# Kernel optimization log

Hardware: AMD Instinct MI355X
Metric: run time of the kernel (lower is better)

Reference implementation:

```python
import jax, jax.numpy as jnp
import numpy as np

DIM = 4096
N_HEADS = 32
N_KV_HEADS = 8
HEAD_DIM = DIM // N_HEADS  # 128
N_REP = N_HEADS // N_KV_HEADS  # 4
THETA = 10000.0
B, S = 4, 1024


def setup_inputs() -> dict:
    key = jax.random.key(0)
    ks = jax.random.split(key, 5)
    sc = 1.0 / np.sqrt(DIM).astype(np.float32)
    x = jax.random.normal(ks[0], (B, S, DIM), jnp.float32)
    wq = jax.random.normal(ks[1], (DIM, N_HEADS * HEAD_DIM), jnp.float32) * sc
    wk = jax.random.normal(ks[2], (DIM, N_KV_HEADS * HEAD_DIM), jnp.float32) * sc
    wv = jax.random.normal(ks[3], (DIM, N_KV_HEADS * HEAD_DIM), jnp.float32) * sc
    wo = jax.random.normal(ks[4], (N_HEADS * HEAD_DIM, DIM), jnp.float32) * sc
    return {"x": x, "wq": wq, "wk": wk, "wv": wv, "wo": wo}


def _rope_cos_sin(seq_len):
    # matches precompute_freqs_cis: freqs over even indices, angles = t * freqs
    freqs = 1.0 / (THETA ** (jnp.arange(0, HEAD_DIM, 2, dtype=jnp.float32) / HEAD_DIM))
    t = jnp.arange(seq_len, dtype=jnp.float32)
    ang = jnp.outer(t, freqs)  # [S, HEAD_DIM//2]
    return jnp.cos(ang), jnp.sin(ang)


def _apply_rope(x, cos, sin):
    # x: [B, S, H, D]; consecutive pairs form complex numbers (view_as_complex)
    xr = x[..., 0::2]
    xi = x[..., 1::2]
    c = cos[None, :, None, :]
    s = sin[None, :, None, :]
    out_r = xr * c - xi * s
    out_i = xr * s + xi * c
    return jnp.stack([out_r, out_i], axis=-1).reshape(x.shape)


def reference(x, wq, wk, wv, wo):
    bsz, seq_len, _ = x.shape
    q = (x @ wq).reshape(bsz, seq_len, N_HEADS, HEAD_DIM)
    k = (x @ wk).reshape(bsz, seq_len, N_KV_HEADS, HEAD_DIM)
    v = (x @ wv).reshape(bsz, seq_len, N_KV_HEADS, HEAD_DIM)
    cos, sin = _rope_cos_sin(seq_len)
    q = _apply_rope(q, cos, sin)
    k = _apply_rope(k, cos, sin)
    # repeat_kv: expand each kv head N_REP times contiguously
    k = jnp.repeat(k, N_REP, axis=2)
    v = jnp.repeat(v, N_REP, axis=2)
    scores = jnp.einsum('bqhd,bkhd->bhqk', q, k) / np.float32(np.sqrt(HEAD_DIM))
    mask = jnp.triu(jnp.full((seq_len, seq_len), -jnp.inf, dtype=scores.dtype), k=1)
    scores = scores + mask
    attn = jax.nn.softmax(scores.astype(jnp.float32), axis=-1).astype(q.dtype)
    out = jnp.einsum('bhqk,bkhd->bqhd', attn, v).reshape(bsz, seq_len, N_HEADS * HEAD_DIM)
    return out @ wo
```

## Files before the change

### kernel.cpp

```cpp
#include <hip/hip_runtime.h>

typedef unsigned short u16;
typedef unsigned int u32;
typedef __attribute__((ext_vector_type(8))) short short8_t;
typedef __attribute__((ext_vector_type(4))) float f32x4;

static constexpr int Bc = 4, Sc = 1024, Hc = 32, HKVc = 8, Dc = 128;
static constexpr int BS = Bc * Sc;
static constexpr int DIMc = 4096;

__device__ __forceinline__ u16 f2bf(float f) {
  u32 u = __float_as_uint(f);
  u32 r = (u + 0x7fffu + ((u >> 16) & 1u)) >> 16;
  return (u16)r;
}
__device__ __forceinline__ float bf2f(u16 u) {
  return __uint_as_float(((u32)u) << 16);
}
__device__ __forceinline__ void gload_lds16(const void* g, void* l) {
  __builtin_amdgcn_global_load_lds((const __attribute__((address_space(1))) void*)g,
                                   (__attribute__((address_space(3))) void*)l, 16, 0, 0);
}

#define SBAR __builtin_amdgcn_sched_barrier(0)
#define PBARRIER do { SBAR; __builtin_amdgcn_s_barrier(); SBAR; } while (0)
#define WAITVM(N) asm volatile("s_waitcnt vmcnt(" #N ")" ::: "memory")

__global__ void rope_table_k(float* __restrict__ tbl) {
  int i = blockIdx.x * 256 + threadIdx.x;
  int s = i >> 6, fi = i & 63;
  float freq = powf(10000.f, -(float)fi / 64.f);
  float ang = (float)s * freq;
  float sv, cv;
  sincosf(ang, &sv, &cv);
  tbl[2 * i] = cv;
  tbl[2 * i + 1] = sv;
}

__global__ void f32_to_bf16_k(const float* __restrict__ in, u16* __restrict__ out, int n4) {
  int i = blockIdx.x * 256 + threadIdx.x;
  if (i >= n4) return;
  float4 v = *(const float4*)(in + (size_t)i * 4);
  uint2 pk;
  pk.x = (u32)f2bf(v.x) | ((u32)f2bf(v.y) << 16);
  pk.y = (u32)f2bf(v.z) | ((u32)f2bf(v.w) << 16);
  *(uint2*)(out + (size_t)i * 4) = pk;
}

__global__ __launch_bounds__(256) void transpose_w_k(const float* __restrict__ W, u16* __restrict__ WT,
                                                     int Kdim, int Ndim) {
  __shared__ float tile[64 * 65];
  const int t = threadIdx.x;
  const int n0 = blockIdx.x * 64, k0 = blockIdx.y * 64;
  #pragma unroll
  for (int p = 0; p < 4; ++p) {
    int idx = p * 256 + t;
    int r = idx >> 4, c = (idx & 15) * 4;
    float4 v = *(const float4*)(W + (size_t)(k0 + r) * Ndim + n0 + c);
    tile[r * 65 + c + 0] = v.x;
    tile[r * 65 + c + 1] = v.y;
    tile[r * 65 + c + 2] = v.z;
    tile[r * 65 + c + 3] = v.w;
  }
  __syncthreads();
  #pragma unroll
  for (int p = 0; p < 2; ++p) {
    int idx = p * 256 + t;
    int n = idx >> 3, c = (idx & 7) * 8;
    alignas(16) u16 o[8];
    #pragma unroll
    for (int i = 0; i < 8; ++i) o[i] = f2bf(tile[(c + i) * 65 + n]);
    *(uint4*)(WT + (size_t)(n0 + n) * Kdim + k0 + c) = *(const uint4*)o;
  }
}

#define MFMAQ(QI, AF, BF)                                                                \
  do {                                                                                   \
    __builtin_amdgcn_s_setprio(1);                                                       \
    _Pragma("unroll") for (int mf = 0; mf < 4; ++mf)                                     \
      _Pragma("unroll") for (int nf = 0; nf < 2; ++nf)                                   \
        _Pragma("unroll") for (int kk = 0; kk < 2; ++kk)                                 \
          acc[QI][mf][nf] = __builtin_amdgcn_mfma_f32_16x16x32_bf16(                     \
              AF[mf][kk], BF[nf][kk], acc[QI][mf][nf], 0, 0, 0);                         \
    __builtin_amdgcn_s_setprio(0);                                                       \
  } while (0)

template <int MODE>
__global__ __launch_bounds__(512, 2) void gemm256(const u16* __restrict__ A, const u16* __restrict__ BT,
                                                  void* __restrict__ Cv, const float* __restrict__ tbl,
                                                  int M, int N, int K) {
  extern __shared__ char smem[];
  const int t = threadIdx.x, l = t & 63, w = t >> 6;
  const int ln15 = l & 15, lh = l >> 4;
  const int NT = K >> 6;

  int id = blockIdx.x;
  int nwg = gridDim.x;
  int swz = ((nwg & 7) == 0) ? ((id & 7) * (nwg >> 3) + (id >> 3)) : id;
  const int nbn = N >> 8;
  const int bm = swz / nbn, bn = swz % nbn;

  const u16* Ag = A + (size_t)bm * 256 * K;
  const u16* Bg = BT + (size_t)bn * 256 * K;

  f32x4 acc[4][4][2];
  #pragma unroll
  for (int q = 0; q < 4; ++q)
    #pragma unroll
    for (int mf = 0; mf < 4; ++mf)
      #pragma unroll
      for (int nf = 0; nf < 2; ++nf) acc[q][mf][nf] = f32x4{0.f, 0.f, 0.f, 0.f};
  short8_t af[4][2], af2[4][2], bfB0[2][2], bfB1[2][2];

  const int srow = (l >> 3);
  const int sck  = (l & 7) ^ srow;
  auto stageA = [&](char* bufbase, int h, int tt) {
    char* lb = bufbase + h * 16384 + w * 1024;
    const u16* g = Ag + (size_t)(h * 128 + w * 8 + srow) * K + tt * 64 + (sck << 3);
    gload_lds16(g, lb);
    gload_lds16(g + (size_t)64 * K, lb + 8192);
  };
  auto stageB = [&](char* bufbase, int h, int tt) {
    char* lb = bufbase + 32768 + h * 16384 + w * 1024;
    const u16* g = Bg + (size_t)(h * 128 + w * 8 + srow) * K + tt * 64 + (sck << 3);
    gload_lds16(g, lb);
    gload_lds16(g + (size_t)64 * K, lb + 8192);
  };
  const int arow = (w >> 2) * 64 + ln15;
  const int brow = (w & 3) * 32 + ln15;
  const int rsw = ln15 & 7;
  auto LDA = [&](const char* cb, int qm, short8_t (&dst)[4][2]) {
    #pragma unroll
    for (int mf = 0; mf < 4; ++mf)
      #pragma unroll
      for (int kk = 0; kk < 2; ++kk)
        dst[mf][kk] = *(const short8_t*)(cb + qm * 16384 + (arow + mf * 16) * 128 +
                                         (((kk * 4 + lh) ^ rsw) << 4));
  };
  auto LDB = [&](const char* cb, int qn, short8_t (&dst)[2][2]) {
    #pragma unroll
    for (int nf = 0; nf < 2; ++nf)
      #pragma unroll
      for (int kk = 0; kk < 2; ++kk)
        dst[nf][kk] = *(const short8_t*)(cb + 32768 + qn * 16384 + (brow + nf * 16) * 128 +
                                         (((kk * 4 + lh) ^ rsw) << 4));
  };

  stageA(smem, 0, 0);
  stageB(smem, 0, 0);
  stageB(smem, 1, 0);
  stageA(smem, 1, 0);
  WAITVM(2);
  PBARRIER;

  for (int T = 0; T < NT; ++T) {
    char* cb = smem + (T & 1) * 65536;
    char* nb = smem + ((T & 1) ^ 1) * 65536;
    const bool s1 = (T + 1 < NT);
    LDB(cb, 0, bfB0);
    LDB(cb, 1, bfB1);
    if (s1) {
      stageA(nb, 0, T + 1);
      stageB(nb, 0, T + 1);
      stageB(nb, 1, T + 1);
      stageA(nb, 1, T + 1);
    }
    LDA(cb, 0, af);
    MFMAQ(0, af, bfB0);
    MFMAQ(3, af, bfB1);
    if (s1) { WAITVM(8); } else { WAITVM(0); }
    LDA(cb, 1, af2);
    MFMAQ(1, af2, bfB0);
    MFMAQ(2, af2, bfB1);
    if (s1) { WAITVM(2); }
    PBARRIER;
  }

  const int rw = (w >> 2) * 64, cw = (w & 3) * 32;
  #pragma unroll
  for (int qi = 0; qi < 4; ++qi) {
    const int qm = (qi == 1 || qi == 2) ? 1 : 0;
    const int qn = (qi >= 2) ? 1 : 0;
    #pragma unroll
    for (int mf = 0; mf < 4; ++mf)
      #pragma unroll
      for (int nf = 0; nf < 2; ++nf)
        #pragma unroll
        for (int e = 0; e < 4; ++e) {
          int row = bm * 256 + qm * 128 + rw + mf * 16 + lh * 4 + e;
          int col = bn * 256 + qn * 128 + cw + nf * 16 + ln15;
          float v = acc[qi][mf][nf][e];
          if (MODE == 2) {
            float pv = __shfl_xor(v, 1);
            int d = col & 127, hh = col >> 7;
            int s = row & (Sc - 1), bb = row >> 10;
            float2 cs = *(const float2*)(tbl + (size_t)(s * 64 + (d >> 1)) * 2);
            float o = (d & 1) ? (v * cs.x + pv * cs.y) : (v * cs.x - pv * cs.y);
            o *= 0.08838834764831845f;
            ((u16*)Cv)[(((size_t)(bb * Hc + hh) * Sc + s) << 7) + d] = f2bf(o);
          } else {
            size_t idx = (size_t)row * N + col;
            ((float*)Cv)[idx] = v;
          }
        }
  }
}

#define MFMAKV(PH, BF)                                                                   \
  do {                                                                                   \
    __builtin_amdgcn_s_setprio(1);                                                       \
    _Pragma("unroll") for (int mf = 0; mf < 4; ++mf)                                     \
      _Pragma("unroll") for (int nf = 0; nf < 2; ++nf)                                   \
        _Pragma("unroll") for (int kk = 0; kk < 2; ++kk)                                 \
          acc[mf][(PH) * 2 + nf] = __builtin_amdgcn_mfma_f32_16x16x32_bf16(              \
              af[mf][kk], BF[nf][kk], acc[mf][(PH) * 2 + nf], 0, 0, 0);                  \
    __builtin_amdgcn_s_setprio(0);                                                       \
  } while (0)

__global__ __launch_bounds__(512, 1) void gemm_kv(const u16* __restrict__ A, const u16* __restrict__ BT,
                                                  u16* __restrict__ Krp, u16* __restrict__ Vtp,
                                                  const float* __restrict__ tbl) {
  extern __shared__ char smem[];
  const int t = threadIdx.x, l = t & 63, w = t >> 6;
  const int ln15 = l & 15, lh = l >> 4;
  const int K = 4096, NT = 64;

  int id = blockIdx.x;
  int swz = (id & 7) * 32 + (id >> 3);
  const int bm = swz >> 3, bn = swz & 7;

  const u16* Ag = A + (size_t)bm * 128 * K;
  const u16* Bg = BT + (size_t)bn * 256 * K;

  f32x4 acc[4][4];
  #pragma unroll
  for (int mf = 0; mf < 4; ++mf)
    #pragma unroll
    for (int nf = 0; nf < 4; ++nf) acc[mf][nf] = f32x4{0.f, 0.f, 0.f, 0.f};
  short8_t af[4][2], bfL[2][2], bfR[2][2];

  const int srow = (l >> 3);
  const int sck  = (l & 7) ^ srow;
  auto stageA = [&](int buf, int tt) {
    char* lb = smem + buf * 16384 + w * 1024;
    const u16* g = Ag + (size_t)(w * 8 + srow) * K + tt * 64 + (sck << 3);
    gload_lds16(g, lb);
    gload_lds16(g + (size_t)64 * K, lb + 8192);
  };
  auto stageB = [&](int buf, int h, int tt) {
    char* lb = smem + 32768 + buf * 32768 + h * 16384 + w * 1024;
    const u16* g = Bg + (size_t)(h * 128 + w * 8 + srow) * K + tt * 64 + (sck << 3);
    gload_lds16(g, lb);
    gload_lds16(g + (size_t)64 * K, lb + 8192);
  };
  const int arow = (w >> 2) * 64 + ln15;
  const int bcol0 = (w & 3) * 64;
  const int rsw = ln15 & 7;
  auto LDA = [&](int buf) {
    #pragma unroll
    for (int mf = 0; mf < 4; ++mf)
      #pragma unroll
      for (int kk = 0; kk < 2; ++kk)
        af[mf][kk] = *(const short8_t*)(smem + buf * 16384 + (arow + mf * 16) * 128 +
                                        (((kk * 4 + lh) ^ rsw) << 4));
  };
  auto LDB = [&](int buf, int half, short8_t (&dst)[2][2]) {
    #pragma unroll
    for (int nf = 0; nf < 2; ++nf)
      #pragma unroll
      for (int kk = 0; kk < 2; ++kk) {
        int brow = bcol0 + (half * 2 + nf) * 16 + ln15;
        dst[nf][kk] = *(const short8_t*)(smem + 32768 + buf * 32768 + brow * 128 +
                                         (((kk * 4 + lh) ^ rsw) << 4));
      }
  };

  stageA(0, 0);
  stageB(0, 0, 0);
  stageB(0, 1, 0);
  WAITVM(2);
  PBARRIER;

  for (int T = 0; T < NT; ++T) {
    const int cb = T & 1, nb = cb ^ 1;
    const bool st = (T + 1 < NT);
    LDA(cb);
    LDB(cb, 0, bfL);
    if (st) { stageA(nb, T + 1); stageB(nb, 0, T + 1); stageB(nb, 1, T + 1); }
    MFMAKV(0, bfL);
    if (st) { WAITVM(6); } else { WAITVM(0); }
    LDB(cb, 1, bfR);
    MFMAKV(1, bfR);
    if (st) { WAITVM(2); }
    PBARRIER;
  }

  #pragma unroll
  for (int mf = 0; mf < 4; ++mf)
    #pragma unroll
    for (int nf = 0; nf < 4; ++nf)
      #pragma unroll
      for (int e = 0; e < 4; ++e) {
        int row = bm * 128 + (w >> 2) * 64 + mf * 16 + lh * 4 + e;
        int col = bn * 256 + bcol0 + nf * 16 + ln15;
        float v = acc[mf][nf][e];
        float pv = __shfl_xor(v, 1);
        int s = row & (Sc - 1), bb = row >> 10;
        if (col < 1024) {
          int hkv = col >> 7, d = col & 127;
          float2 cs = *(const float2*)(tbl + (size_t)(s * 64 + (d >> 1)) * 2);
          float o = (d & 1) ? (v * cs.x + pv * cs.y) : (v * cs.x - pv * cs.y);
          Krp[(((size_t)(bb * HKVc + hkv) * Sc + s) << 7) + d] = f2bf(o);
        } else {
          int vc = col - 1024;
          int hkv = vc >> 7, d = vc & 127;
          int sl = s & 63;
          int sg = (sl & 32) | (((sl >> 2) & 3) << 3) | (((sl >> 4) & 1) << 2) | (sl & 3);
          Vtp[((size_t)(bb * HKVc + hkv) * Dc + d) * Sc + (s & ~63) + sg] = f2bf(v);
        }
      }
}

__global__ __launch_bounds__(512, 4) void attn_k(const u16* __restrict__ Q, const u16* __restrict__ Kr,
                                                 const u16* __restrict__ Vt, u16* __restrict__ AO) {
  extern __shared__ char smem[];
  const int t = threadIdx.x, l = t & 63, w = t >> 6;
  const int qb = (int)gridDim.x - 1 - (int)blockIdx.x;
  const int h = blockIdx.y, b = blockIdx.z;
  const int hkv = h >> 2;
  const int ln15 = l & 15, lh = l >> 4;
  const int NT = 2 * qb + 2;

  const u16* Kg0 = Kr + (size_t)(b * HKVc + hkv) * Sc * Dc;
  const u16* Vg0 = Vt + (size_t)(b * HKVc + hkv) * Dc * Sc;

  auto stageK = [&](int buf, int tt) {
    char* base = smem + buf * 16384 + w * 2048;
    #pragma unroll
    for (int i = 0; i < 2; ++i) {
      int row = w * 8 + i * 4 + (l >> 4);
      int c = l & 15;
      gload_lds16(Kg0 + (size_t)(tt * 64 + row) * Dc + ((c ^ (row & 7)) << 3), base + i * 1024);
    }
  };
  auto stageV = [&](int buf, int tt) {
    char* base = smem + 32768 + buf * 16384 + w * 2048;
    #pragma unroll
    for (int i = 0; i < 2; ++i) {
      int d = w * 16 + i * 8 + (l >> 3);
      int c = l & 7;
      gload_lds16(Vg0 + (size_t)d * Sc + tt * 64 + ((c ^ (d & 7)) << 3), base + i * 1024);
    }
  };

  short8_t qf[4];
  {
    int q = qb * 128 + w * 16 + ln15;
    const u16* qp = Q + ((size_t)(b * Hc + h) * Sc + q) * Dc + lh * 8;
    #pragma unroll
    for (int ks = 0; ks < 4; ++ks) qf[ks] = *(const short8_t*)(qp + ks * 32);
  }
  SBAR;

  f32x4 oacc[8];
  #pragma unroll
  for (int i = 0; i < 8; ++i) oacc[i] = f32x4{0.f, 0.f, 0.f, 0.f};
  float mrun = -1e30f, lrun = 0.f;

  stageK(0, 0); stageV(0, 0);
  stageK(1, 1); stageV(1, 1);

  const int qmaxw = qb * 128 + w * 16 + 15;
  const int qlane = qb * 128 + w * 16 + ln15;

  for (int T = 0; T < NT; ++T) {
    if (T < NT - 1) { WAITVM(4); } else { WAITVM(0); }
    PBARRIER;
    const char* Kb = smem + (T & 1) * 16384;
    const char* Vb = smem + 32768 + (T & 1) * 16384;

    if (T * 64 <= qmaxw) {
      f32x4 sf[4];
      #pragma unroll
      for (int fc = 0; fc < 4; ++fc) {
        sf[fc] = f32x4{0.f, 0.f, 0.f, 0.f};
        int kvr = fc * 16 + ln15;
        #pragma unroll
        for (int ks = 0; ks < 4; ++ks) {
          int chunk = ks * 4 + lh;
          short8_t kf = *(const short8_t*)(Kb + kvr * 256 + ((chunk ^ (kvr & 7)) << 4));
          sf[fc] = __builtin_amdgcn_mfma_f32_16x16x32_bf16(kf, qf[ks], sf[fc], 0, 0, 0);
        }
      }
      if (T * 64 + 63 > qb * 128 + w * 16) {
        #pragma unroll
        for (int fc = 0; fc < 4; ++fc)
          #pragma unroll
          for (int j = 0; j < 4; ++j) {
            int kvg = T * 64 + fc * 16 + lh * 4 + j;
            if (kvg > qlane) sf[fc][j] = -1e30f;
          }
      }
      float mx = sf[0][0];
      #pragma unroll
      for (int fc = 0; fc < 4; ++fc)
        #pragma unroll
        for (int j = 0; j < 4; ++j) mx = fmaxf(mx, sf[fc][j]);
      mx = fmaxf(mx, __shfl_xor(mx, 16));
      mx = fmaxf(mx, __shfl_xor(mx, 32));
      float mnew = fmaxf(mrun, mx);
      float alpha = __expf(mrun - mnew);
      mrun = mnew;
      float rs = 0.f;
      #pragma unroll
      for (int fc = 0; fc < 4; ++fc)
        #pragma unroll
        for (int j = 0; j < 4; ++j) {
          float p = __expf(sf[fc][j] - mnew);
          sf[fc][j] = p;
          rs += p;
        }
      rs += __shfl_xor(rs, 16);
      rs += __shfl_xor(rs, 32);
      lrun = lrun * alpha + rs;
      float arow[4];
      #pragma unroll
      for (int j = 0; j < 4; ++j) arow[j] = __shfl(alpha, (l & 48) | (lh * 4 + j));
      #pragma unroll
      for (int fd = 0; fd < 8; ++fd)
        #pragma unroll
        for (int j = 0; j < 4; ++j) oacc[fd][j] *= arow[j];
      short8_t pa[2];
      #pragma unroll
      for (int ks = 0; ks < 2; ++ks)
        #pragma unroll
        for (int b2 = 0; b2 < 2; ++b2)
          #pragma unroll
          for (int j = 0; j < 4; ++j) pa[ks][b2 * 4 + j] = (short)f2bf(sf[ks * 2 + b2][j]);
      #pragma unroll
      for (int fd = 0; fd < 8; ++fd) {
        int dcol = fd * 16 + ln15;
        #pragma unroll
        for (int ks = 0; ks < 2; ++ks) {
          int chunk = ks * 4 + lh;
          short8_t vf = *(const short8_t*)(Vb + dcol * 128 + ((chunk ^ (dcol & 7)) << 4));
          oacc[fd] = __builtin_amdgcn_mfma_f32_16x16x32_bf16(pa[ks], vf, oacc[fd], 0, 0, 0);
        }
      }
    }
    PBARRIER;
    if (T + 2 < NT) { stageK(T & 1, T + 2); stageV(T & 1, T + 2); }
  }

  float linv[4];
  #pragma unroll
  for (int j = 0; j < 4; ++j) linv[j] = 1.f / __shfl(lrun, (l & 48) | (lh * 4 + j));
  #pragma unroll
  for (int j = 0; j < 4; ++j) {
    int q = qb * 128 + w * 16 + lh * 4 + j;
    u16* op = AO + (size_t)(b * Sc + q) * DIMc + h * Dc + ln15;
    #pragma unroll
    for (int fd = 0; fd < 8; ++fd) op[fd * 16] = f2bf(oacc[fd][j] * linv[j]);
  }
}

extern "C" void kernel_launch(void* const* d_in, const int* in_sizes, int n_in,
                              void* d_out, int out_size, void* d_ws, size_t ws_size,
                              hipStream_t stream) {
  const float* x  = (const float*)d_in[0];
  const float* wq = (const float*)d_in[1];
  const float* wk = (const float*)d_in[2];
  const float* wv = (const float*)d_in[3];
  const float* wo = (const float*)d_in[4];
  float* out = (float*)d_out;

  char* ws = (char*)d_ws;
  size_t off = 0;
  auto alloc = [&](size_t bytes) -> char* {
    char* p = ws + off;
    off += (bytes + 255) & ~(size_t)255;
    return p;
  };
  float* tbl  = (float*)alloc((size_t)Sc * 64 * 2 * 4);
  u16* xb    = (u16*)alloc((size_t)BS * DIMc * 2);
  u16* wqT   = (u16*)alloc((size_t)4096 * 4096 * 2);
  u16* wkvT  = (u16*)alloc((size_t)2048 * 4096 * 2);
  u16* Qb    = (u16*)alloc((size_t)BS * 4096 * 2);
  u16* Krp   = (u16*)alloc((size_t)BS * 1024 * 2);
  u16* Vtp   = (u16*)alloc((size_t)BS * 1024 * 2);
  u16* AO = xb;
  u16* woT = wqT;

  rope_table_k<<<(Sc * 64) / 256, 256, 0, stream>>>(tbl);
  f32_to_bf16_k<<<(BS * DIMc / 4) / 256, 256, 0, stream>>>(x, xb, BS * DIMc / 4);

  transpose_w_k<<<dim3(64, 64), 256, 0, stream>>>(wq, wqT, 4096, 4096);
  gemm256<2><<<256, 512, 131072, stream>>>(xb, wqT, Qb, tbl, 4096, 4096, 4096);

  transpose_w_k<<<dim3(16, 64), 256, 0, stream>>>(wk, wkvT, 4096, 1024);
  transpose_w_k<<<dim3(16, 64), 256, 0, stream>>>(wv, wkvT + (size_t)1024 * 4096, 4096, 1024);
  gemm_kv<<<256, 512, 98304, stream>>>(xb, wkvT, Krp, Vtp, tbl);

  attn_k<<<dim3(8, Hc, Bc), 512, 65536, stream>>>(Qb, Krp, Vtp, AO);

  transpose_w_k<<<dim3(64, 64), 256, 0, stream>>>(wo, woT, 4096, 4096);
  gemm256<1><<<256, 512, 131072, stream>>>(AO, woT, out, tbl, 4096, 4096, 4096);
}
```

Measured before the change: 470.8 us.

## Process two query row groups per wave in attention to reuse K/V fragments

The attention kernel now runs with 4 waves of 256 threads instead of 8, and each wave handles 32 query rows as two 16-row groups. Each K and V fragment read from LDS feeds two MFMAs, which halves LDS reads per unit of compute. Each thread now stages twice as many K/V chunks, and the vmcnt wait is adjusted to match. The cost is higher register pressure, fewer waves per block to hide latency, and coarser causal skipping because whole 32-row wave spans are gated together.

```diff
diff --git a/kernel.cpp b/kernel.cpp
--- a/kernel.cpp
+++ b/kernel.cpp
@@ -321,7 +321,7 @@
       }
 }
 
-__global__ __launch_bounds__(512, 4) void attn_k(const u16* __restrict__ Q, const u16* __restrict__ Kr,
+__global__ __launch_bounds__(256, 2) void attn_k(const u16* __restrict__ Q, const u16* __restrict__ Kr,
                                                  const u16* __restrict__ Vt, u16* __restrict__ AO) {
   extern __shared__ char smem[];
   const int t = threadIdx.x, l = t & 63, w = t >> 6;
@@ -335,108 +335,119 @@
   const u16* Vg0 = Vt + (size_t)(b * HKVc + hkv) * Dc * Sc;
 
   auto stageK = [&](int buf, int tt) {
-    char* base = smem + buf * 16384 + w * 2048;
-    #pragma unroll
-    for (int i = 0; i < 2; ++i) {
-      int row = w * 8 + i * 4 + (l >> 4);
+    char* base = smem + buf * 16384 + w * 4096;
+    #pragma unroll
+    for (int i = 0; i < 4; ++i) {
+      int row = w * 16 + i * 4 + (l >> 4);
       int c = l & 15;
       gload_lds16(Kg0 + (size_t)(tt * 64 + row) * Dc + ((c ^ (row & 7)) << 3), base + i * 1024);
     }
   };
   auto stageV = [&](int buf, int tt) {
-    char* base = smem + 32768 + buf * 16384 + w * 2048;
-    #pragma unroll
-    for (int i = 0; i < 2; ++i) {
-      int d = w * 16 + i * 8 + (l >> 3);
+    char* base = smem + 32768 + buf * 16384 + w * 4096;
+    #pragma unroll
+    for (int i = 0; i < 4; ++i) {
+      int d = w * 32 + i * 8 + (l >> 3);
       int c = l & 7;
       gload_lds16(Vg0 + (size_t)d * Sc + tt * 64 + ((c ^ (d & 7)) << 3), base + i * 1024);
     }
   };
 
-  short8_t qf[4];
-  {
-    int q = qb * 128 + w * 16 + ln15;
+  short8_t qf[2][4];
+  #pragma unroll
+  for (int g = 0; g < 2; ++g) {
+    int q = qb * 128 + w * 32 + g * 16 + ln15;
     const u16* qp = Q + ((size_t)(b * Hc + h) * Sc + q) * Dc + lh * 8;
     #pragma unroll
-    for (int ks = 0; ks < 4; ++ks) qf[ks] = *(const short8_t*)(qp + ks * 32);
+    for (int ks = 0; ks < 4; ++ks) qf[g][ks] = *(const short8_t*)(qp + ks * 32);
   }
   SBAR;
 
-  f32x4 oacc[8];
-  #pragma unroll
-  for (int i = 0; i < 8; ++i) oacc[i] = f32x4{0.f, 0.f, 0.f, 0.f};
-  float mrun = -1e30f, lrun = 0.f;
+  f32x4 oacc[2][8];
+  #pragma unroll
+  for (int g = 0; g < 2; ++g)
+    #pragma unroll
+    for (int i = 0; i < 8; ++i) oacc[g][i] = f32x4{0.f, 0.f, 0.f, 0.f};
+  float mrun[2] = {-1e30f, -1e30f}, lrun[2] = {0.f, 0.f};
 
   stageK(0, 0); stageV(0, 0);
   stageK(1, 1); stageV(1, 1);
 
-  const int qmaxw = qb * 128 + w * 16 + 15;
-  const int qlane = qb * 128 + w * 16 + ln15;
+  const int qmaxw = qb * 128 + w * 32 + 31;
 
   for (int T = 0; T < NT; ++T) {
-    if (T < NT - 1) { WAITVM(4); } else { WAITVM(0); }
+    if (T < NT - 1) { WAITVM(8); } else { WAITVM(0); }
     PBARRIER;
     const char* Kb = smem + (T & 1) * 16384;
     const char* Vb = smem + 32768 + (T & 1) * 16384;
 
     if (T * 64 <= qmaxw) {
-      f32x4 sf[4];
+      f32x4 sf[2][4];
       #pragma unroll
       for (int fc = 0; fc < 4; ++fc) {
-        sf[fc] = f32x4{0.f, 0.f, 0.f, 0.f};
+        sf[0][fc] = f32x4{0.f, 0.f, 0.f, 0.f};
+        sf[1][fc] = f32x4{0.f, 0.f, 0.f, 0.f};
         int kvr = fc * 16 + ln15;
         #pragma unroll
         for (int ks = 0; ks < 4; ++ks) {
           int chunk = ks * 4 + lh;
           short8_t kf = *(const short8_t*)(Kb + kvr * 256 + ((chunk ^ (kvr & 7)) << 4));
-          sf[fc] = __builtin_amdgcn_mfma_f32_16x16x32_bf16(kf, qf[ks], sf[fc], 0, 0, 0);
+          sf[0][fc] = __builtin_amdgcn_mfma_f32_16x16x32_bf16(kf, qf[0][ks], sf[0][fc], 0, 0, 0);
+          sf[1][fc] = __builtin_amdgcn_mfma_f32_16x16x32_bf16(kf, qf[1][ks], sf[1][fc], 0, 0, 0);
         }
       }
-      if (T * 64 + 63 > qb * 128 + w * 16) {
+      if (T * 64 + 63 > qb * 128 + w * 32) {
+        #pragma unroll
+        for (int g = 0; g < 2; ++g) {
+          int qlane = qb * 128 + w * 32 + g * 16 + ln15;
+          #pragma unroll
+          for (int fc = 0; fc < 4; ++fc)
+            #pragma unroll
+            for (int j = 0; j < 4; ++j) {
+              int kvg = T * 64 + fc * 16 + lh * 4 + j;
+              if (kvg > qlane) sf[g][fc][j] = -1e30f;
+            }
+        }
+      }
+      short8_t pa[2][2];
+      #pragma unroll
+      for (int g = 0; g < 2; ++g) {
+        float mx = sf[g][0][0];
+        #pragma unroll
+        for (int fc = 0; fc < 4; ++fc)
+          #pragma unroll
+          for (int j = 0; j < 4; ++j) mx = fmaxf(mx, sf[g][fc][j]);
+        mx = fmaxf(mx, __shfl_xor(mx, 16));
+        mx = fmaxf(mx, __shfl_xor(mx, 32));
+        float mnew = fmaxf(mrun[g], mx);
+        float alpha = __expf(mrun[g] - mnew);
+        mrun[g] = mnew;
+        float rs = 0.f;
         #pragma unroll
         for (int fc = 0; fc < 4; ++fc)
           #pragma unroll
           for (int j = 0; j < 4; ++j) {
-            int kvg = T * 64 + fc * 16 + lh * 4 + j;
-            if (kvg > qlane) sf[fc][j] = -1e30f;
+            float p = __expf(sf[g][fc][j] - mnew);
+            sf[g][fc][j] = p;
+            rs += p;
           }
+        rs += __shfl_xor(rs, 16);
+        rs += __shfl_xor(rs, 32);
+        lrun[g] = lrun[g] * alpha + rs;
+        float arow[4];
+        #pragma unroll
+        for (int j = 0; j < 4; ++j) arow[j] = __shfl(alpha, (l & 48) | (lh * 4 + j));
+        #pragma unroll
+        for (int fd = 0; fd < 8; ++fd)
+          #pragma unroll
+          for (int j = 0; j < 4; ++j) oacc[g][fd][j] *= arow[j];
+        #pragma unroll
+        for (int ks = 0; ks < 2; ++ks)
+          #pragma unroll
+          for (int b2 = 0; b2 < 2; ++b2)
+            #pragma unroll
+            for (int j = 0; j < 4; ++j) pa[g][ks][b2 * 4 + j] = (short)f2bf(sf[g][ks * 2 + b2][j]);
       }
-      float mx = sf[0][0];
-      #pragma unroll
-      for (int fc = 0; fc < 4; ++fc)
-        #pragma unroll
-        for (int j = 0; j < 4; ++j) mx = fmaxf(mx, sf[fc][j]);
-      mx = fmaxf(mx, __shfl_xor(mx, 16));
-      mx = fmaxf(mx, __shfl_xor(mx, 32));
-      float mnew = fmaxf(mrun, mx);
-      float alpha = __expf(mrun - mnew);
-      mrun = mnew;
-      float rs = 0.f;
-      #pragma unroll
-      for (int fc = 0; fc < 4; ++fc)
-        #pragma unroll
-        for (int j = 0; j < 4; ++j) {
-          float p = __expf(sf[fc][j] - mnew);
-          sf[fc][j] = p;
-          rs += p;
-        }
-      rs += __shfl_xor(rs, 16);
-      rs += __shfl_xor(rs, 32);
-      lrun = lrun * alpha + rs;
-      float arow[4];
-      #pragma unroll
-      for (int j = 0; j < 4; ++j) arow[j] = __shfl(alpha, (l & 48) | (lh * 4 + j));
-      #pragma unroll
-      for (int fd = 0; fd < 8; ++fd)
-        #pragma unroll
-        for (int j = 0; j < 4; ++j) oacc[fd][j] *= arow[j];
-      short8_t pa[2];
-      #pragma unroll
-      for (int ks = 0; ks < 2; ++ks)
-        #pragma unroll
-        for (int b2 = 0; b2 < 2; ++b2)
-          #pragma unroll
-          for (int j = 0; j < 4; ++j) pa[ks][b2 * 4 + j] = (short)f2bf(sf[ks * 2 + b2][j]);
       #pragma unroll
       for (int fd = 0; fd < 8; ++fd) {
         int dcol = fd * 16 + ln15;
@@ -444,7 +455,8 @@
         for (int ks = 0; ks < 2; ++ks) {
           int chunk = ks * 4 + lh;
           short8_t vf = *(const short8_t*)(Vb + dcol * 128 + ((chunk ^ (dcol & 7)) << 4));
-          oacc[fd] = __builtin_amdgcn_mfma_f32_16x16x32_bf16(pa[ks], vf, oacc[fd], 0, 0, 0);
+          oacc[0][fd] = __builtin_amdgcn_mfma_f32_16x16x32_bf16(pa[0][ks], vf, oacc[0][fd], 0, 0, 0);
+          oacc[1][fd] = __builtin_amdgcn_mfma_f32_16x16x32_bf16(pa[1][ks], vf, oacc[1][fd], 0, 0, 0);
         }
       }
     }
@@ -452,15 +464,18 @@
     if (T + 2 < NT) { stageK(T & 1, T + 2); stageV(T & 1, T + 2); }
   }
 
-  float linv[4];
-  #pragma unroll
-  for (int j = 0; j < 4; ++j) linv[j] = 1.f / __shfl(lrun, (l & 48) | (lh * 4 + j));
-  #pragma unroll
-  for (int j = 0; j < 4; ++j) {
-    int q = qb * 128 + w * 16 + lh * 4 + j;
-    u16* op = AO + (size_t)(b * Sc + q) * DIMc + h * Dc + ln15;
-    #pragma unroll
-    for (int fd = 0; fd < 8; ++fd) op[fd * 16] = f2bf(oacc[fd][j] * linv[j]);
+  #pragma unroll
+  for (int g = 0; g < 2; ++g) {
+    float linv[4];
+    #pragma unroll
+    for (int j = 0; j < 4; ++j) linv[j] = 1.f / __shfl(lrun[g], (l & 48) | (lh * 4 + j));
+    #pragma unroll
+    for (int j = 0; j < 4; ++j) {
+      int q = qb * 128 + w * 32 + g * 16 + lh * 4 + j;
+      u16* op = AO + (size_t)(b * Sc + q) * DIMc + h * Dc + ln15;
+      #pragma unroll
+      for (int fd = 0; fd < 8; ++fd) op[fd * 16] = f2bf(oacc[g][fd][j] * linv[j]);
+    }
   }
 }
 
@@ -501,7 +516,7 @@
   transpose_w_k<<<dim3(16, 64), 256, 0, stream>>>(wv, wkvT + (size_t)1024 * 4096, 4096, 1024);
   gemm_kv<<<256, 512, 98304, stream>>>(xb, wkvT, Krp, Vtp, tbl);
 
-  attn_k<<<dim3(8, Hc, Bc), 512, 65536, stream>>>(Qb, Krp, Vtp, AO);
+  attn_k<<<dim3(8, Hc, Bc), 256, 65536, stream>>>(Qb, Krp, Vtp, AO);
 
   transpose_w_k<<<dim3(64, 64), 256, 0, stream>>>(wo, woT, 4096, 4096);
   gemm256<1><<<256, 512, 131072, stream>>>(AO, woT, out, tbl, 4096, 4096, 4096);
```

After: 468.7 us. Within noise of the previous version (-0.4%).
